# Kernel optimization log

Measured on AMD Instinct MI355X. Metric: run time of the kernel, lower is better.

Reference implementation:

```python
import jax, jax.numpy as jnp
import numpy as np
import math

B, T, D_IN, D_OUT = 2, 2048, 4096, 4096
N_HEADS, N_KV = 32, 8
HEAD_DIM = D_OUT // N_HEADS  # 128
GROUP_SIZE = N_HEADS // N_KV  # 4
ROPE_BASE = 500000.0
CTX = 2048


def _rope_tables(head_dim, base, seq_len):
    inv_freq = 1.0 / base ** (jnp.arange(0, head_dim, 2, dtype=jnp.float32) / head_dim)
    t = jnp.arange(seq_len, dtype=jnp.float32)
    freqs = jnp.einsum('i,j->ij', t, inv_freq)  # (T, head_dim/2)
    return jnp.cos(freqs), jnp.sin(freqs)


def _apply_rope(x, cos, sin):
    # x: (B, H, T, Dh); cos/sin: (T, Dh/2)
    x1, x2 = jnp.split(x, 2, axis=-1)
    c = cos[None, None]
    s = sin[None, None]
    return jnp.concatenate([x1 * c - x2 * s, x1 * s + x2 * c], axis=-1)


def setup_inputs() -> dict:
    key = jax.random.key(0)
    ks = jax.random.split(key, 5)
    scale = 0.02
    return {
        'x': jax.random.normal(ks[0], (B, T, D_IN), dtype=jnp.float32),
        'Wq': jax.random.normal(ks[1], (D_IN, D_OUT), dtype=jnp.float32) * scale,
        'Wk': jax.random.normal(ks[2], (D_IN, N_KV * HEAD_DIM), dtype=jnp.float32) * scale,
        'Wv': jax.random.normal(ks[3], (D_IN, N_KV * HEAD_DIM), dtype=jnp.float32) * scale,
        'Wo': jax.random.normal(ks[4], (D_OUT, D_OUT), dtype=jnp.float32) * scale,
    }


def reference(x, Wq, Wk, Wv, Wo):
    b, t, _ = x.shape
    cos, sin = _rope_tables(HEAD_DIM, ROPE_BASE, t)  # start_pos = 0

    q = (x @ Wq).reshape(b, t, N_HEADS, HEAD_DIM).transpose(0, 2, 1, 3)  # (B,H,T,Dh)
    k = (x @ Wk).reshape(b, t, N_KV, HEAD_DIM).transpose(0, 2, 1, 3)    # (B,G,T,Dh)
    v = (x @ Wv).reshape(b, t, N_KV, HEAD_DIM).transpose(0, 2, 1, 3)    # (B,G,T,Dh)

    q = _apply_rope(q, cos, sin)
    k = _apply_rope(k, cos, sin)

    # GQA: repeat_interleave KV groups to match query heads
    k_h = jnp.repeat(k, GROUP_SIZE, axis=1)  # (B,H,T,Dh)
    v_h = jnp.repeat(v, GROUP_SIZE, axis=1)

    scores = jnp.einsum('bhqd,bhkd->bhqk', q, k_h) / math.sqrt(HEAD_DIM)
    causal = jnp.triu(jnp.ones((t, t), dtype=bool), k=1)
    scores = jnp.where(causal[None, None], jnp.finfo(scores.dtype).min, scores)
    attn = jax.nn.softmax(scores, axis=-1)

    ctx = jnp.einsum('bhqk,bhkd->bhqd', attn, v_h)           # (B,H,T,Dh)
    ctx = ctx.transpose(0, 2, 1, 3).reshape(b, t, D_OUT)     # (B,T,D)
    return ctx @ Wo
```

## Files before the change

kernel.cpp:

```cpp
#include <hip/hip_runtime.h>
#include <hip/hip_bf16.h>

#define T_SEQ 2048
#define NH 32
#define NKV 8
#define DH 128

typedef unsigned short u16;
typedef __attribute__((ext_vector_type(8))) short short8;
typedef __attribute__((ext_vector_type(4))) float floatx4;

union U8 { u16 s[8]; uint4 v; };

__device__ inline u16 f2bf(float f) {
  __hip_bfloat16 h = __float2bfloat16(f);
  return *reinterpret_cast<u16*>(&h);
}
__device__ inline float bf2f(u16 u) {
  __hip_bfloat16 h;
  *reinterpret_cast<u16*>(&h) = u;
  return __bfloat162float(h);
}

__device__ inline void store_out(float* p, float v) { *p = v; }
__device__ inline void store_out(u16* p, float v) { *p = f2bf(v); }

#define GLD_LDS(g, l) __builtin_amdgcn_global_load_lds( \
    (const __attribute__((address_space(1))) void*)(g), \
    (__attribute__((address_space(3))) void*)(l), 16, 0, 0)

__global__ void cast_x_kernel(const float* __restrict__ in, u16* __restrict__ out, int n8) {
  int idx = blockIdx.x * blockDim.x + threadIdx.x;
  if (idx >= n8) return;
  const float4* p = reinterpret_cast<const float4*>(in) + (size_t)idx * 2;
  float4 f0 = p[0], f1 = p[1];
  U8 u;
  u.s[0] = f2bf(f0.x); u.s[1] = f2bf(f0.y); u.s[2] = f2bf(f0.z); u.s[3] = f2bf(f0.w);
  u.s[4] = f2bf(f1.x); u.s[5] = f2bf(f1.y); u.s[6] = f2bf(f1.z); u.s[7] = f2bf(f1.w);
  *reinterpret_cast<uint4*>(out + (size_t)idx * 8) = u.v;
}

__global__ void transpose_cast_kernel(const float* __restrict__ W, u16* __restrict__ WT,
                                      int K, int N) {
  __shared__ u16 tile[64][72];
  int tid = threadIdx.x;
  int n0 = blockIdx.x * 64, k0 = blockIdx.y * 64;
  int r = tid >> 2, seg = (tid & 3) * 16;
  const float* wp = W + (size_t)(k0 + r) * N + n0 + seg;
#pragma unroll
  for (int jj = 0; jj < 4; ++jj) {
    float4 f = *(const float4*)(wp + jj * 4);
    tile[r][seg + jj * 4 + 0] = f2bf(f.x);
    tile[r][seg + jj * 4 + 1] = f2bf(f.y);
    tile[r][seg + jj * 4 + 2] = f2bf(f.z);
    tile[r][seg + jj * 4 + 3] = f2bf(f.w);
  }
  __syncthreads();
  u16* op = WT + (size_t)(n0 + r) * K + k0 + seg;
#pragma unroll
  for (int jj = 0; jj < 4; ++jj) {
    ushort4 o;
    o.x = tile[seg + jj * 4 + 0][r];
    o.y = tile[seg + jj * 4 + 1][r];
    o.z = tile[seg + jj * 4 + 2][r];
    o.w = tile[seg + jj * 4 + 3][r];
    *(ushort4*)(op + jj * 4) = o;
  }
}

__global__ void rope_kernel(u16* __restrict__ qkv) {
  int idx = blockIdx.x * blockDim.x + threadIdx.x;
  int i = idx & 63;
  int head = (idx >> 6) % 40;
  int row = idx / (64 * 40);
  int t = row & (T_SEQ - 1);
  int col = head < 32 ? head * 128 : 4096 + (head - 32) * 128;
  size_t base = (size_t)row * 6144 + col;
  float x1 = bf2f(qkv[base + i]);
  float x2 = bf2f(qkv[base + 64 + i]);
  float inv = exp2f(-(float)i * (18.931568569324174f / 64.0f));
  float ang = (float)t * inv;
  float c = cosf(ang), s = sinf(ang);
  qkv[base + i]      = f2bf(x1 * c - x2 * s);
  qkv[base + 64 + i] = f2bf(x1 * s + x2 * c);
}

__global__ void vtrans_kernel(const u16* __restrict__ qkv, u16* __restrict__ vt) {
  __shared__ u16 tile[64][72];
  int tid = threadIdx.x;
  int t0 = blockIdx.x * 64, d0 = blockIdx.y * 64, bg = blockIdx.z;
  int b = bg >> 3, g = bg & 7;
  int r = tid >> 2, seg = (tid & 3) * 16;
  const u16* src = qkv + (size_t)(b * T_SEQ + t0 + r) * 6144 + 5120 + g * 128 + d0 + seg;
  *(uint4*)&tile[r][seg] = *(const uint4*)src;
  *(uint4*)&tile[r][seg + 8] = *(const uint4*)(src + 8);
  __syncthreads();
  u16* dst = vt + (size_t)(bg * 128 + d0 + r) * T_SEQ + t0 + seg;
  U8 o0, o1;
#pragma unroll
  for (int e = 0; e < 8; ++e) o0.s[e] = tile[seg + e][r];
#pragma unroll
  for (int e = 0; e < 8; ++e) o1.s[e] = tile[seg + 8 + e][r];
  *(uint4*)dst = o0.v;
  *(uint4*)(dst + 8) = o1.v;
}

template <typename OutT>
__global__ __launch_bounds__(256) void gemm_bt(const u16* __restrict__ A,
                                               const u16* __restrict__ B,
                                               OutT* __restrict__ C,
                                               int M, int N, int Kd, int ldc) {
  __shared__ u16 As[128 * 64];
  __shared__ u16 Bs[128 * 64];
  int tid = threadIdx.x;
  int wave = tid >> 6, lane = tid & 63;
  int l15 = lane & 15, quad = lane >> 4;
  int wr = wave >> 1, wc = wave & 1;
  int m0 = blockIdx.y * 128, n0 = blockIdx.x * 128;

  floatx4 acc[4][4];
#pragma unroll
  for (int mt = 0; mt < 4; ++mt)
#pragma unroll
    for (int nt = 0; nt < 4; ++nt)
#pragma unroll
      for (int r = 0; r < 4; ++r) acc[mt][nt][r] = 0.0f;

  int rloc = lane >> 3, slot = lane & 7;
  const u16* agp = A + (size_t)(m0 + wave * 32 + rloc) * Kd + ((slot ^ rloc) * 8);
  const u16* bgp = B + (size_t)(n0 + wave * 32 + rloc) * Kd + ((slot ^ rloc) * 8);
  u16* alp = As + (wave * 32) * 64;
  u16* blp = Bs + (wave * 32) * 64;

  for (int kt = 0; kt < Kd; kt += 64) {
    __syncthreads();
#pragma unroll
    for (int j = 0; j < 4; ++j) {
      GLD_LDS(agp + kt + (size_t)j * 8 * Kd, alp + j * 8 * 64);
      GLD_LDS(bgp + kt + (size_t)j * 8 * Kd, blp + j * 8 * 64);
    }
    __syncthreads();
#pragma unroll
    for (int ks = 0; ks < 2; ++ks) {
      short8 af[4], bfr[4];
      int sl = ((ks * 4 + quad) ^ (l15 & 7)) * 8;
#pragma unroll
      for (int mt = 0; mt < 4; ++mt)
        af[mt] = *(const short8*)&As[(wr * 64 + mt * 16 + l15) * 64 + sl];
#pragma unroll
      for (int nt = 0; nt < 4; ++nt)
        bfr[nt] = *(const short8*)&Bs[(wc * 64 + nt * 16 + l15) * 64 + sl];
#pragma unroll
      for (int mt = 0; mt < 4; ++mt)
#pragma unroll
        for (int nt = 0; nt < 4; ++nt)
          acc[mt][nt] = __builtin_amdgcn_mfma_f32_16x16x32_bf16(af[mt], bfr[nt], acc[mt][nt], 0, 0, 0);
    }
  }

#pragma unroll
  for (int mt = 0; mt < 4; ++mt)
#pragma unroll
    for (int nt = 0; nt < 4; ++nt)
#pragma unroll
      for (int r = 0; r < 4; ++r) {
        int rr = m0 + wr * 64 + mt * 16 + quad * 4 + r;
        int cc = n0 + wc * 64 + nt * 16 + l15;
        store_out(&C[(size_t)rr * ldc + cc], acc[mt][nt][r]);
      }
}

__global__ __launch_bounds__(256) void attn_kernel(const u16* __restrict__ qkv,
                                                   const u16* __restrict__ vt,
                                                   u16* __restrict__ CTX) {
  const int bx = (gridDim.x - 1) - blockIdx.x;
  const int bh = blockIdx.y;
  const int b = bh >> 5, h = bh & 31;
  const int g = h >> 2;
  const int bg = b * NKV + g;
  const int tid = threadIdx.x;
  const int w = tid >> 6, lane = tid & 63;
  const int l15 = lane & 15, quad = lane >> 4;
  const int q0 = bx * 128;

  __shared__ u16 Ks[64 * 128];
  __shared__ u16 Vs[128 * 64];
  __shared__ u16 Ps[4][32 * 72];

  short8 aq[2][4];
#pragma unroll
  for (int mf = 0; mf < 2; ++mf) {
    int qrow = q0 + w * 32 + mf * 16 + l15;
    const u16* qp = qkv + (size_t)(b * T_SEQ + qrow) * 6144 + h * 128;
#pragma unroll
    for (int ks = 0; ks < 4; ++ks)
      aq[mf][ks] = *(const short8*)(qp + ks * 32 + quad * 8);
  }

  float m_r[2][4], ell[2][4];
  floatx4 o[2][8];
#pragma unroll
  for (int mf = 0; mf < 2; ++mf)
#pragma unroll
    for (int r = 0; r < 4; ++r) { m_r[mf][r] = -1e30f; ell[mf][r] = 0.0f; }
#pragma unroll
  for (int mf = 0; mf < 2; ++mf)
#pragma unroll
    for (int dt = 0; dt < 8; ++dt)
#pragma unroll
      for (int r = 0; r < 4; ++r) o[mf][dt][r] = 0.0f;

  const float scale = 0.08838834764831845f;
  const int ntiles = 2 * bx + 2;

  const int krloc = lane >> 4, kslot = lane & 15;
  const int vrloc = lane >> 3, vslot = lane & 7;
  const u16* kbase = qkv + (size_t)(b * T_SEQ) * 6144 + 4096 + g * 128;
  const u16* vbase = vt + (size_t)(bg * 128) * T_SEQ;

  for (int kt = 0; kt < ntiles; ++kt) {
    const int k0 = kt * 64;
    __syncthreads();
#pragma unroll
    for (int j = 0; j < 4; ++j) {
      int rk = w * 16 + j * 4 + krloc;
      int gck = (kslot & 8) | ((kslot & 7) ^ (rk & 7));
      GLD_LDS(kbase + (size_t)(k0 + rk) * 6144 + gck * 8, Ks + (w * 16 + j * 4) * 128);
      int rv = w * 32 + j * 8 + vrloc;
      int gcv = vslot ^ vrloc;
      GLD_LDS(vbase + (size_t)rv * T_SEQ + k0 + gcv * 8, Vs + (w * 32 + j * 8) * 64);
    }
    __syncthreads();

    if (k0 > q0 + w * 32 + 31) continue;

    floatx4 sacc[2][4];
#pragma unroll
    for (int mf = 0; mf < 2; ++mf)
#pragma unroll
      for (int nt = 0; nt < 4; ++nt)
#pragma unroll
        for (int r = 0; r < 4; ++r) sacc[mf][nt][r] = 0.0f;
#pragma unroll
    for (int ks = 0; ks < 4; ++ks) {
      int c = ks * 4 + quad;
      int sl = ((c & 8) | ((c & 7) ^ (l15 & 7))) * 8;
#pragma unroll
      for (int nt = 0; nt < 4; ++nt) {
        short8 bk = *(const short8*)&Ks[(nt * 16 + l15) * 128 + sl];
        sacc[0][nt] = __builtin_amdgcn_mfma_f32_16x16x32_bf16(aq[0][ks], bk, sacc[0][nt], 0, 0, 0);
        sacc[1][nt] = __builtin_amdgcn_mfma_f32_16x16x32_bf16(aq[1][ks], bk, sacc[1][nt], 0, 0, 0);
      }
    }

#pragma unroll
    for (int mf = 0; mf < 2; ++mf) {
      const int rowbase = q0 + w * 32 + mf * 16;
      float s[4][4];
#pragma unroll
      for (int nt = 0; nt < 4; ++nt)
#pragma unroll
        for (int r = 0; r < 4; ++r) s[nt][r] = sacc[mf][nt][r] * scale;

      if (k0 + 63 > rowbase) {
#pragma unroll
        for (int nt = 0; nt < 4; ++nt) {
          int col = k0 + nt * 16 + l15;
#pragma unroll
          for (int r = 0; r < 4; ++r) {
            int row = rowbase + quad * 4 + r;
            if (col > row) s[nt][r] = -1e30f;
          }
        }
      }

      float alpha[4];
#pragma unroll
      for (int r = 0; r < 4; ++r) {
        float m = fmaxf(fmaxf(s[0][r], s[1][r]), fmaxf(s[2][r], s[3][r]));
        m = fmaxf(m, __shfl_xor(m, 1));
        m = fmaxf(m, __shfl_xor(m, 2));
        m = fmaxf(m, __shfl_xor(m, 4));
        m = fmaxf(m, __shfl_xor(m, 8));
        float mnew = fmaxf(m_r[mf][r], m);
        alpha[r] = __expf(m_r[mf][r] - mnew);
        m_r[mf][r] = mnew;
      }
      float rsum[4];
#pragma unroll
      for (int r = 0; r < 4; ++r) {
        float acc_s = 0.0f;
#pragma unroll
        for (int nt = 0; nt < 4; ++nt) {
          float p = __expf(s[nt][r] - m_r[mf][r]);
          s[nt][r] = p;
          acc_s += p;
        }
        acc_s += __shfl_xor(acc_s, 1);
        acc_s += __shfl_xor(acc_s, 2);
        acc_s += __shfl_xor(acc_s, 4);
        acc_s += __shfl_xor(acc_s, 8);
        rsum[r] = acc_s;
      }
#pragma unroll
      for (int r = 0; r < 4; ++r) ell[mf][r] = ell[mf][r] * alpha[r] + rsum[r];
#pragma unroll
      for (int dt = 0; dt < 8; ++dt)
#pragma unroll
        for (int r = 0; r < 4; ++r) o[mf][dt][r] *= alpha[r];

#pragma unroll
      for (int nt = 0; nt < 4; ++nt)
#pragma unroll
        for (int r = 0; r < 4; ++r)
          Ps[w][(mf * 16 + quad * 4 + r) * 72 + nt * 16 + l15] = f2bf(s[nt][r]);
    }

    short8 pf[2][2];
#pragma unroll
    for (int mf = 0; mf < 2; ++mf)
#pragma unroll
      for (int ks2 = 0; ks2 < 2; ++ks2)
        pf[mf][ks2] = *(const short8*)&Ps[w][(mf * 16 + l15) * 72 + ks2 * 32 + quad * 8];

#pragma unroll
    for (int dt = 0; dt < 8; ++dt) {
#pragma unroll
      for (int ks2 = 0; ks2 < 2; ++ks2) {
        int sl = (((ks2 * 4 + quad) ^ (l15 & 7))) * 8;
        short8 bv = *(const short8*)&Vs[(dt * 16 + l15) * 64 + sl];
        o[0][dt] = __builtin_amdgcn_mfma_f32_16x16x32_bf16(pf[0][ks2], bv, o[0][dt], 0, 0, 0);
        o[1][dt] = __builtin_amdgcn_mfma_f32_16x16x32_bf16(pf[1][ks2], bv, o[1][dt], 0, 0, 0);
      }
    }
  }

#pragma unroll
  for (int mf = 0; mf < 2; ++mf) {
    float inv_l[4];
#pragma unroll
    for (int r = 0; r < 4; ++r) inv_l[r] = 1.0f / ell[mf][r];
#pragma unroll
    for (int dt = 0; dt < 8; ++dt)
#pragma unroll
      for (int r = 0; r < 4; ++r) {
        int row = q0 + w * 32 + mf * 16 + quad * 4 + r;
        CTX[(size_t)(b * T_SEQ + row) * 4096 + h * 128 + dt * 16 + l15] =
            f2bf(o[mf][dt][r] * inv_l[r]);
      }
  }
}

extern "C" void kernel_launch(void* const* d_in, const int* in_sizes, int n_in,
                              void* d_out, int out_size, void* d_ws, size_t ws_size,
                              hipStream_t stream) {
  const float* x  = (const float*)d_in[0];
  const float* Wq = (const float*)d_in[1];
  const float* Wk = (const float*)d_in[2];
  const float* Wv = (const float*)d_in[3];
  const float* Wo = (const float*)d_in[4];
  float* out = (float*)d_out;

  char* ws = (char*)d_ws;
  const size_t SZ_X    = (size_t)4096 * 4096 * 2;
  const size_t SZ_QKVW = (size_t)6144 * 4096 * 2;
  u16* xb    = (u16*)(ws);
  u16* wqkvT = (u16*)(ws + SZ_X);
  u16* woT   = (u16*)(ws + SZ_X + SZ_QKVW);
  u16* qkv   = (u16*)(ws + SZ_X + SZ_QKVW + SZ_X);
  u16* vt    = (u16*)(ws + SZ_X + SZ_QKVW + SZ_X + SZ_QKVW);
  u16* ctx   = xb;

  cast_x_kernel<<<8192, 256, 0, stream>>>(x, xb, 2097152);
  transpose_cast_kernel<<<dim3(64, 64), 256, 0, stream>>>(Wq, wqkvT, 4096, 4096);
  transpose_cast_kernel<<<dim3(16, 64), 256, 0, stream>>>(Wk, wqkvT + (size_t)4096 * 4096, 4096, 1024);
  transpose_cast_kernel<<<dim3(16, 64), 256, 0, stream>>>(Wv, wqkvT + (size_t)5120 * 4096, 4096, 1024);
  transpose_cast_kernel<<<dim3(64, 64), 256, 0, stream>>>(Wo, woT, 4096, 4096);

  gemm_bt<u16><<<dim3(48, 32), 256, 0, stream>>>(xb, wqkvT, qkv, 4096, 6144, 4096, 6144);

  rope_kernel<<<40960, 256, 0, stream>>>(qkv);

  vtrans_kernel<<<dim3(32, 2, 16), 256, 0, stream>>>(qkv, vt);

  attn_kernel<<<dim3(16, 64), 256, 0, stream>>>(qkv, vt, ctx);

  gemm_bt<float><<<dim3(32, 32), 256, 0, stream>>>(ctx, woT, out, 4096, 4096, 4096, 4096);
}
```

Baseline: 1.043 ms.

## Restructure attention: paired causal tiles, double-buffered K/V, transposed scores without LDS

Each block now handles a pair of 64-row query tiles (lo and 31-lo) so every block does the same amount of causal work. K/V tiles are double-buffered in LDS with prefetch of the next tile. Scores are computed transposed (K as the A operand), so each lane owns one query row; softmax reductions drop to two cross-quad shuffles, and P is moved into MFMA operand layout with shuffles instead of an LDS round trip. Output stores are vectorized. The cost is more shuffles, LDS doubled to 64KB, which may limit occupancy, and more complex control flow.

Measured after the change: 919.6 us. 1.13x faster.

```diff
diff --git a/kernel.cpp b/kernel.cpp
--- a/kernel.cpp
+++ b/kernel.cpp
@@ -7,10 +7,12 @@
 #define DH 128
 
 typedef unsigned short u16;
+typedef unsigned int u32;
 typedef __attribute__((ext_vector_type(8))) short short8;
 typedef __attribute__((ext_vector_type(4))) float floatx4;
 
 union U8 { u16 s[8]; uint4 v; };
+union F8 { u32 d[4]; short8 s; };
 
 __device__ inline u16 f2bf(float f) {
   __hip_bfloat16 h = __float2bfloat16(f);
@@ -170,10 +172,83 @@
       }
 }
 
+__device__ inline void softmax_pv(floatx4* sc, float& m_s, float& ell_s,
+                                  floatx4* o, const u16* Vsb,
+                                  int qglob, int k0, bool diag,
+                                  int l15, int quad) {
+  const float scale = 0.08838834764831845f;
+  float s[4][4];
+#pragma unroll
+  for (int t4 = 0; t4 < 4; ++t4)
+#pragma unroll
+    for (int r = 0; r < 4; ++r) {
+      float v = sc[t4][r] * scale;
+      if (diag && (k0 + t4 * 16 + quad * 4 + r > qglob)) v = -1e30f;
+      s[t4][r] = v;
+    }
+  float m = s[0][0];
+#pragma unroll
+  for (int t4 = 0; t4 < 4; ++t4)
+#pragma unroll
+    for (int r = 0; r < 4; ++r) m = fmaxf(m, s[t4][r]);
+  m = fmaxf(m, __shfl_xor(m, 16));
+  m = fmaxf(m, __shfl_xor(m, 32));
+  float mnew = fmaxf(m_s, m);
+  float alpha = __expf(m_s - mnew);
+  m_s = mnew;
+  float sum = 0.f;
+#pragma unroll
+  for (int t4 = 0; t4 < 4; ++t4)
+#pragma unroll
+    for (int r = 0; r < 4; ++r) {
+      float p = __expf(s[t4][r] - mnew);
+      s[t4][r] = p;
+      sum += p;
+    }
+  sum += __shfl_xor(sum, 16);
+  sum += __shfl_xor(sum, 32);
+  ell_s = ell_s * alpha + sum;
+#pragma unroll
+  for (int dt = 0; dt < 8; ++dt)
+#pragma unroll
+    for (int r = 0; r < 4; ++r) o[dt][r] *= alpha;
+
+  u32 pk[4][2];
+#pragma unroll
+  for (int t4 = 0; t4 < 4; ++t4) {
+    pk[t4][0] = (u32)f2bf(s[t4][0]) | ((u32)f2bf(s[t4][1]) << 16);
+    pk[t4][1] = (u32)f2bf(s[t4][2]) | ((u32)f2bf(s[t4][3]) << 16);
+  }
+  int sidxA = (2 * (quad & 1)) * 16 + l15;
+  int sidxB = sidxA + 16;
+  bool hiq = (quad & 2) != 0;
+  F8 pf[2];
+#pragma unroll
+  for (int h = 0; h < 2; ++h) {
+    u32 a0 = __shfl((int)pk[2 * h][0], sidxA), b0 = __shfl((int)pk[2 * h + 1][0], sidxA);
+    u32 a1 = __shfl((int)pk[2 * h][1], sidxA), b1 = __shfl((int)pk[2 * h + 1][1], sidxA);
+    u32 a2 = __shfl((int)pk[2 * h][0], sidxB), b2 = __shfl((int)pk[2 * h + 1][0], sidxB);
+    u32 a3 = __shfl((int)pk[2 * h][1], sidxB), b3 = __shfl((int)pk[2 * h + 1][1], sidxB);
+    pf[h].d[0] = hiq ? b0 : a0;
+    pf[h].d[1] = hiq ? b1 : a1;
+    pf[h].d[2] = hiq ? b2 : a2;
+    pf[h].d[3] = hiq ? b3 : a3;
+  }
+  int sl0 = ((0 + quad) ^ (l15 & 7)) * 8;
+  int sl1 = ((4 + quad) ^ (l15 & 7)) * 8;
+#pragma unroll
+  for (int dt = 0; dt < 8; ++dt) {
+    short8 va0 = *(const short8*)&Vsb[(dt * 16 + l15) * 64 + sl0];
+    short8 va1 = *(const short8*)&Vsb[(dt * 16 + l15) * 64 + sl1];
+    o[dt] = __builtin_amdgcn_mfma_f32_16x16x32_bf16(va0, pf[0].s, o[dt], 0, 0, 0);
+    o[dt] = __builtin_amdgcn_mfma_f32_16x16x32_bf16(va1, pf[1].s, o[dt], 0, 0, 0);
+  }
+}
+
 __global__ __launch_bounds__(256) void attn_kernel(const u16* __restrict__ qkv,
                                                    const u16* __restrict__ vt,
                                                    u16* __restrict__ CTX) {
-  const int bx = (gridDim.x - 1) - blockIdx.x;
+  const int bx = blockIdx.x;
   const int bh = blockIdx.y;
   const int b = bh >> 5, h = bh & 31;
   const int g = h >> 2;
@@ -181,173 +256,127 @@
   const int tid = threadIdx.x;
   const int w = tid >> 6, lane = tid & 63;
   const int l15 = lane & 15, quad = lane >> 4;
-  const int q0 = bx * 128;
-
-  __shared__ u16 Ks[64 * 128];
-  __shared__ u16 Vs[128 * 64];
-  __shared__ u16 Ps[4][32 * 72];
+  const int lo = bx, hi = 31 - bx;
+  const int niter = hi + 1;
+
+  __shared__ u16 Ks[2 * 64 * 128];
+  __shared__ u16 Vs[2 * 128 * 64];
+
+  const u16* kbase = qkv + (size_t)(b * T_SEQ) * 6144 + 4096 + g * 128;
+  const u16* vbase = vt + (size_t)(bg * 128) * T_SEQ;
 
   short8 aq[2][4];
-#pragma unroll
-  for (int mf = 0; mf < 2; ++mf) {
-    int qrow = q0 + w * 32 + mf * 16 + l15;
-    const u16* qp = qkv + (size_t)(b * T_SEQ + qrow) * 6144 + h * 128;
-#pragma unroll
-    for (int ks = 0; ks < 4; ++ks)
-      aq[mf][ks] = *(const short8*)(qp + ks * 32 + quad * 8);
-  }
-
-  float m_r[2][4], ell[2][4];
+  const int qg_lo = lo * 64 + w * 16 + l15;
+  const int qg_hi = hi * 64 + w * 16 + l15;
+  {
+    const u16* qp0 = qkv + (size_t)(b * T_SEQ + qg_lo) * 6144 + h * 128;
+    const u16* qp1 = qkv + (size_t)(b * T_SEQ + qg_hi) * 6144 + h * 128;
+#pragma unroll
+    for (int ks = 0; ks < 4; ++ks) {
+      aq[0][ks] = *(const short8*)(qp0 + ks * 32 + quad * 8);
+      aq[1][ks] = *(const short8*)(qp1 + ks * 32 + quad * 8);
+    }
+  }
+
+  float m_s[2] = {-1e30f, -1e30f}, ell[2] = {0.f, 0.f};
   floatx4 o[2][8];
 #pragma unroll
-  for (int mf = 0; mf < 2; ++mf)
-#pragma unroll
-    for (int r = 0; r < 4; ++r) { m_r[mf][r] = -1e30f; ell[mf][r] = 0.0f; }
-#pragma unroll
-  for (int mf = 0; mf < 2; ++mf)
+  for (int t = 0; t < 2; ++t)
 #pragma unroll
     for (int dt = 0; dt < 8; ++dt)
 #pragma unroll
-      for (int r = 0; r < 4; ++r) o[mf][dt][r] = 0.0f;
-
-  const float scale = 0.08838834764831845f;
-  const int ntiles = 2 * bx + 2;
+      for (int r = 0; r < 4; ++r) o[t][dt][r] = 0.0f;
 
   const int krloc = lane >> 4, kslot = lane & 15;
   const int vrloc = lane >> 3, vslot = lane & 7;
-  const u16* kbase = qkv + (size_t)(b * T_SEQ) * 6144 + 4096 + g * 128;
-  const u16* vbase = vt + (size_t)(bg * 128) * T_SEQ;
-
-  for (int kt = 0; kt < ntiles; ++kt) {
-    const int k0 = kt * 64;
-    __syncthreads();
+
+  {
 #pragma unroll
     for (int j = 0; j < 4; ++j) {
       int rk = w * 16 + j * 4 + krloc;
       int gck = (kslot & 8) | ((kslot & 7) ^ (rk & 7));
-      GLD_LDS(kbase + (size_t)(k0 + rk) * 6144 + gck * 8, Ks + (w * 16 + j * 4) * 128);
+      GLD_LDS(kbase + (size_t)rk * 6144 + gck * 8, Ks + (w * 16 + j * 4) * 128);
       int rv = w * 32 + j * 8 + vrloc;
       int gcv = vslot ^ vrloc;
-      GLD_LDS(vbase + (size_t)rv * T_SEQ + k0 + gcv * 8, Vs + (w * 32 + j * 8) * 64);
-    }
+      GLD_LDS(vbase + (size_t)rv * 2048 + gcv * 8, Vs + (w * 32 + j * 8) * 64);
+    }
+  }
+
+  for (int kt = 0; kt < niter; ++kt) {
+    const int buf = kt & 1;
+    const int k0 = kt * 64;
     __syncthreads();
 
-    if (k0 > q0 + w * 32 + 31) continue;
-
-    floatx4 sacc[2][4];
-#pragma unroll
-    for (int mf = 0; mf < 2; ++mf)
-#pragma unroll
-      for (int nt = 0; nt < 4; ++nt)
-#pragma unroll
-        for (int r = 0; r < 4; ++r) sacc[mf][nt][r] = 0.0f;
-#pragma unroll
-    for (int ks = 0; ks < 4; ++ks) {
-      int c = ks * 4 + quad;
-      int sl = ((c & 8) | ((c & 7) ^ (l15 & 7))) * 8;
-#pragma unroll
-      for (int nt = 0; nt < 4; ++nt) {
-        short8 bk = *(const short8*)&Ks[(nt * 16 + l15) * 128 + sl];
-        sacc[0][nt] = __builtin_amdgcn_mfma_f32_16x16x32_bf16(aq[0][ks], bk, sacc[0][nt], 0, 0, 0);
-        sacc[1][nt] = __builtin_amdgcn_mfma_f32_16x16x32_bf16(aq[1][ks], bk, sacc[1][nt], 0, 0, 0);
+    if (kt + 1 < niter) {
+      const int nb = buf ^ 1;
+      const int k0n = k0 + 64;
+#pragma unroll
+      for (int j = 0; j < 4; ++j) {
+        int rk = w * 16 + j * 4 + krloc;
+        int gck = (kslot & 8) | ((kslot & 7) ^ (rk & 7));
+        GLD_LDS(kbase + (size_t)(k0n + rk) * 6144 + gck * 8,
+                Ks + nb * 8192 + (w * 16 + j * 4) * 128);
+        int rv = w * 32 + j * 8 + vrloc;
+        int gcv = vslot ^ vrloc;
+        GLD_LDS(vbase + (size_t)rv * 2048 + k0n + gcv * 8,
+                Vs + nb * 8192 + (w * 32 + j * 8) * 64);
       }
     }
 
-#pragma unroll
-    for (int mf = 0; mf < 2; ++mf) {
-      const int rowbase = q0 + w * 32 + mf * 16;
-      float s[4][4];
-#pragma unroll
-      for (int nt = 0; nt < 4; ++nt)
-#pragma unroll
-        for (int r = 0; r < 4; ++r) s[nt][r] = sacc[mf][nt][r] * scale;
-
-      if (k0 + 63 > rowbase) {
-#pragma unroll
-        for (int nt = 0; nt < 4; ++nt) {
-          int col = k0 + nt * 16 + l15;
-#pragma unroll
-          for (int r = 0; r < 4; ++r) {
-            int row = rowbase + quad * 4 + r;
-            if (col > row) s[nt][r] = -1e30f;
-          }
+    const u16* Ksb = Ks + buf * 8192;
+    const u16* Vsb = Vs + buf * 8192;
+    const bool lo_on = (kt <= lo);
+
+    floatx4 s0[4], s1[4];
+#pragma unroll
+    for (int t4 = 0; t4 < 4; ++t4)
+#pragma unroll
+      for (int r = 0; r < 4; ++r) { s0[t4][r] = 0.f; s1[t4][r] = 0.f; }
+
+    if (lo_on) {
+#pragma unroll
+      for (int ks = 0; ks < 4; ++ks) {
+        int c = ks * 4 + quad;
+        int sl = ((c & 8) | ((c & 7) ^ (l15 & 7))) * 8;
+#pragma unroll
+        for (int t4 = 0; t4 < 4; ++t4) {
+          short8 bk = *(const short8*)&Ksb[(t4 * 16 + l15) * 128 + sl];
+          s1[t4] = __builtin_amdgcn_mfma_f32_16x16x32_bf16(bk, aq[1][ks], s1[t4], 0, 0, 0);
+          s0[t4] = __builtin_amdgcn_mfma_f32_16x16x32_bf16(bk, aq[0][ks], s0[t4], 0, 0, 0);
         }
       }
-
-      float alpha[4];
-#pragma unroll
-      for (int r = 0; r < 4; ++r) {
-        float m = fmaxf(fmaxf(s[0][r], s[1][r]), fmaxf(s[2][r], s[3][r]));
-        m = fmaxf(m, __shfl_xor(m, 1));
-        m = fmaxf(m, __shfl_xor(m, 2));
-        m = fmaxf(m, __shfl_xor(m, 4));
-        m = fmaxf(m, __shfl_xor(m, 8));
-        float mnew = fmaxf(m_r[mf][r], m);
-        alpha[r] = __expf(m_r[mf][r] - mnew);
-        m_r[mf][r] = mnew;
+    } else {
+#pragma unroll
+      for (int ks = 0; ks < 4; ++ks) {
+        int c = ks * 4 + quad;
+        int sl = ((c & 8) | ((c & 7) ^ (l15 & 7))) * 8;
+#pragma unroll
+        for (int t4 = 0; t4 < 4; ++t4) {
+          short8 bk = *(const short8*)&Ksb[(t4 * 16 + l15) * 128 + sl];
+          s1[t4] = __builtin_amdgcn_mfma_f32_16x16x32_bf16(bk, aq[1][ks], s1[t4], 0, 0, 0);
+        }
       }
-      float rsum[4];
-#pragma unroll
-      for (int r = 0; r < 4; ++r) {
-        float acc_s = 0.0f;
-#pragma unroll
-        for (int nt = 0; nt < 4; ++nt) {
-          float p = __expf(s[nt][r] - m_r[mf][r]);
-          s[nt][r] = p;
-          acc_s += p;
-        }
-        acc_s += __shfl_xor(acc_s, 1);
-        acc_s += __shfl_xor(acc_s, 2);
-        acc_s += __shfl_xor(acc_s, 4);
-        acc_s += __shfl_xor(acc_s, 8);
-        rsum[r] = acc_s;
-      }
-#pragma unroll
-      for (int r = 0; r < 4; ++r) ell[mf][r] = ell[mf][r] * alpha[r] + rsum[r];
-#pragma unroll
-      for (int dt = 0; dt < 8; ++dt)
-#pragma unroll
-        for (int r = 0; r < 4; ++r) o[mf][dt][r] *= alpha[r];
-
-#pragma unroll
-      for (int nt = 0; nt < 4; ++nt)
-#pragma unroll
-        for (int r = 0; r < 4; ++r)
-          Ps[w][(mf * 16 + quad * 4 + r) * 72 + nt * 16 + l15] = f2bf(s[nt][r]);
-    }
-
-    short8 pf[2][2];
-#pragma unroll
-    for (int mf = 0; mf < 2; ++mf)
-#pragma unroll
-      for (int ks2 = 0; ks2 < 2; ++ks2)
-        pf[mf][ks2] = *(const short8*)&Ps[w][(mf * 16 + l15) * 72 + ks2 * 32 + quad * 8];
-
+    }
+
+    softmax_pv(s1, m_s[1], ell[1], o[1], Vsb, qg_hi, k0, kt == hi, l15, quad);
+    if (lo_on)
+      softmax_pv(s0, m_s[0], ell[0], o[0], Vsb, qg_lo, k0, kt == lo, l15, quad);
+  }
+
+#pragma unroll
+  for (int t = 0; t < 2; ++t) {
+    float inv_l = 1.0f / ell[t];
+    int qglob = (t ? qg_hi : qg_lo);
+    u16* cp = CTX + (size_t)(b * T_SEQ + qglob) * 4096 + h * 128 + quad * 4;
 #pragma unroll
     for (int dt = 0; dt < 8; ++dt) {
-#pragma unroll
-      for (int ks2 = 0; ks2 < 2; ++ks2) {
-        int sl = (((ks2 * 4 + quad) ^ (l15 & 7))) * 8;
-        short8 bv = *(const short8*)&Vs[(dt * 16 + l15) * 64 + sl];
-        o[0][dt] = __builtin_amdgcn_mfma_f32_16x16x32_bf16(pf[0][ks2], bv, o[0][dt], 0, 0, 0);
-        o[1][dt] = __builtin_amdgcn_mfma_f32_16x16x32_bf16(pf[1][ks2], bv, o[1][dt], 0, 0, 0);
-      }
-    }
-  }
-
-#pragma unroll
-  for (int mf = 0; mf < 2; ++mf) {
-    float inv_l[4];
-#pragma unroll
-    for (int r = 0; r < 4; ++r) inv_l[r] = 1.0f / ell[mf][r];
-#pragma unroll
-    for (int dt = 0; dt < 8; ++dt)
-#pragma unroll
-      for (int r = 0; r < 4; ++r) {
-        int row = q0 + w * 32 + mf * 16 + quad * 4 + r;
-        CTX[(size_t)(b * T_SEQ + row) * 4096 + h * 128 + dt * 16 + l15] =
-            f2bf(o[mf][dt][r] * inv_l[r]);
-      }
+      ushort4 pkd;
+      pkd.x = f2bf(o[t][dt][0] * inv_l);
+      pkd.y = f2bf(o[t][dt][1] * inv_l);
+      pkd.z = f2bf(o[t][dt][2] * inv_l);
+      pkd.w = f2bf(o[t][dt][3] * inv_l);
+      *(ushort4*)(cp + dt * 16) = pkd;
+    }
   }
 }
 
@@ -380,7 +409,6 @@
   gemm_bt<u16><<<dim3(48, 32), 256, 0, stream>>>(xb, wqkvT, qkv, 4096, 6144, 4096, 6144);
 
   rope_kernel<<<40960, 256, 0, stream>>>(qkv);
-
   vtrans_kernel<<<dim3(32, 2, 16), 256, 0, stream>>>(qkv, vt);
 
   attn_kernel<<<dim3(16, 64), 256, 0, stream>>>(qkv, vt, ctx);
```
